# Optimization experiments

Hardware: AMD Instinct MI355X
Metric: run time of the kernel (lower is better)

Reference implementation:

```python
import jax, jax.numpy as jnp
import numpy as np


def setup_inputs() -> dict:
    key = jax.random.key(0)
    k1, k2 = jax.random.split(key)
    x = jax.random.normal(k1, (16, 1024, 512), dtype=jnp.float32)
    embedding = jax.random.normal(k2, (8192, 512), dtype=jnp.float32)
    return {"x": x, "embedding": embedding}


def reference(x, embedding):
    # x: [b, n, c], embedding (codebook k): [m, c]
    b, n, c = x.shape
    m = embedding.shape[0]
    q = x.reshape(b * n, c)            # (b n) c
    k = embedding
    # Squared L2 distance: ||q||^2 + ||k||^2 - 2 q.k  -> [bn, m]
    sim = (jnp.sum(q * q, axis=1, keepdims=True)
           + jnp.sum(k * k, axis=1)
           - 2.0 * jnp.einsum('nc,mc->nm', q, k))
    z_indices = jnp.argmin(sim, axis=1)                     # [bn]
    z_onehot = jax.nn.one_hot(z_indices, m, dtype=jnp.float32)  # [bn, m]
    # Direct gather is mathematically identical to onehot @ k
    z = k[z_indices]                                        # [bn, c]
    # Straight-through estimator: z = q + sg(z - q)
    z_st = q + jax.lax.stop_gradient(z - q)
    # Perplexity of code usage
    z_mean = jnp.mean(z_onehot, axis=0)                     # [m]
    perplexity = jnp.exp(-jnp.sum(z_mean * jnp.log(z_mean + 1e-10)))
    return (z_st.reshape(b, n, c),
            z_indices.reshape(b, n),
            z_onehot.reshape(b, n, m),
            perplexity)
```

## Files before the change

### kernel.cpp

```cpp
#include <hip/hip_runtime.h>
#include <cstdint>
#include <cstddef>

#define BNR 16384
#define C   512
#define M   8192
#define BM  128
#define BN  128
#define BK  64
#define NCH 8
#define NSETS 64

#define NZERO 512
#define GEMM_BLOCKS 8192
#define OH4_PER_ZB  65536

#define TILE_U16   8192
#define PANEL_U16  65536

typedef float f32x4 __attribute__((ext_vector_type(4)));
typedef _Float16 f16x8 __attribute__((ext_vector_type(8)));
typedef unsigned short u16;

static __device__ __forceinline__ u16 h_bits(_Float16 h) {
    union { _Float16 h; u16 u; } x; x.h = h; return x.u;
}
static __device__ __forceinline__ void gl_lds16(const void* g, void* l) {
    __builtin_amdgcn_global_load_lds(
        (const __attribute__((address_space(1))) void*)g,
        (__attribute__((address_space(3))) void*)l, 16, 0, 0);
}

__global__ void knorm_k(const float* __restrict__ emb, float* __restrict__ knorm) {
    int gw   = (blockIdx.x * blockDim.x + threadIdx.x) >> 6;
    int lane = threadIdx.x & 63;
    int nw   = (gridDim.x * blockDim.x) >> 6;
    for (int row = gw; row < M; row += nw) {
        const float4* p = (const float4*)(emb + (size_t)row * C);
        float s = 0.f;
#pragma unroll
        for (int j = 0; j < 2; ++j) {
            float4 v = p[lane + 64 * j];
            s += v.x * v.x + v.y * v.y + v.z * v.z + v.w * v.w;
        }
#pragma unroll
        for (int o = 32; o > 0; o >>= 1) s += __shfl_down(s, o, 64);
        if (lane == 0) knorm[row] = s;
    }
}

__global__ void cvt_tile_k(const float* __restrict__ in, u16* __restrict__ outp) {
    int o = blockIdx.x * 256 + threadIdx.x;
    int q = o & 1023, kb = q >> 7, row = q & 127;
    int c = (o >> 10) & 7, pan = o >> 13;
    int grow = pan * BM + row;
    int k0 = c * BK + kb * 8;
    const float4* src = (const float4*)(in + (size_t)grow * C + k0);
    float4 a = src[0], b = src[1];
    u16 v[8] = { h_bits((_Float16)a.x), h_bits((_Float16)a.y),
                 h_bits((_Float16)a.z), h_bits((_Float16)a.w),
                 h_bits((_Float16)b.x), h_bits((_Float16)b.y),
                 h_bits((_Float16)b.z), h_bits((_Float16)b.w) };
    u16* dst = outp + (size_t)o * 8;
    *(ushort4*)(dst)     = *(ushort4*)(v);
    *(ushort4*)(dst + 4) = *(ushort4*)(v + 4);
}

__global__ void mega_k(
    const u16* __restrict__ x2t, const u16* __restrict__ e2t,
    const float* __restrict__ knorm,
    float* __restrict__ pv1, int* __restrict__ pi1,
    float* __restrict__ pv2, int* __restrict__ pi2,
    float* __restrict__ onehot) {
    __shared__ __align__(16) u16 ldsA[8][128][8];
    __shared__ __align__(16) u16 ldsB[8][128][8];

    if (blockIdx.x < NZERO) {
        f32x4* o4 = (f32x4*)onehot;
        size_t base = (size_t)blockIdx.x * OH4_PER_ZB + threadIdx.x;
        const f32x4 z = (f32x4)(0.0f);
#pragma unroll 4
        for (int i = 0; i < OH4_PER_ZB / 256; ++i)
            __builtin_nontemporal_store(z, &o4[base + (size_t)i * 256]);
        return;
    }

    const int gid  = blockIdx.x - NZERO;
    const int tid  = threadIdx.x;
    const int lane = tid & 63;
    const int w    = tid >> 6;
    const int wm   = w >> 1, wn = w & 1;
    const int g    = lane >> 4, r = lane & 15;

    const int xk = gid & 7, j = gid >> 3;
    const int stid = (j >> 6) * 8 + xk;
    const int p  = j & 63;
    const int rb = (stid & 15) * 8 + (p & 7);
    const int cb = (stid >> 4) * 8 + (p >> 3);
    const int rowBase = rb * BM, colBase = cb * BN;

    f32x4 acc[4][4];
#pragma unroll
    for (int m = 0; m < 4; ++m)
#pragma unroll
        for (int n = 0; n < 4; ++n) acc[m][n] = (f32x4)(0.0f);

    const u16* aT = x2t + (size_t)rb * PANEL_U16;
    const u16* bT = e2t + (size_t)cb * PANEL_U16;

#pragma unroll 1
    for (int c = 0; c < NCH; ++c) {
        if (c) __syncthreads();
#pragma unroll
        for (int it = 0; it < 4; ++it) {
            int u = it * 256 + tid;
            gl_lds16(aT + (size_t)c * TILE_U16 + u * 8, (u16*)ldsA + u * 8);
            gl_lds16(bT + (size_t)c * TILE_U16 + u * 8, (u16*)ldsB + u * 8);
        }
        __syncthreads();

#pragma unroll
        for (int ks = 0; ks < 2; ++ks) {
            const int kb = ks * 4 + g;
            f16x8 a[4], b[4];
#pragma unroll
            for (int m = 0; m < 4; ++m)
                a[m] = *(const f16x8*)&ldsA[kb][wm * 64 + m * 16 + r][0];
#pragma unroll
            for (int n = 0; n < 4; ++n)
                b[n] = *(const f16x8*)&ldsB[kb][wn * 64 + n * 16 + r][0];
#pragma unroll
            for (int m = 0; m < 4; ++m)
#pragma unroll
                for (int n = 0; n < 4; ++n)
                    acc[m][n] = __builtin_amdgcn_mfma_f32_16x16x32_f16(
                        a[m], b[n], acc[m][n], 0, 0, 0);
        }
    }
    __syncthreads();

    float kn[4];
#pragma unroll
    for (int n = 0; n < 4; ++n) kn[n] = knorm[colBase + wn * 64 + n * 16 + r];

    float* mv = (float*)&ldsA[0][0][0];
    int*   mi = (int*)(mv + 2 * 128 * 2);

#pragma unroll
    for (int m = 0; m < 4; ++m) {
#pragma unroll
        for (int q = 0; q < 4; ++q) {
            float v1 = 3.0e38f, v2 = 3.0e38f;
            int   i1 = 0x7fffffff, i2 = 0x7fffffff;
#pragma unroll
            for (int n = 0; n < 4; ++n) {
                int col = colBase + wn * 64 + n * 16 + r;
                float d = fmaf(-2.0f, acc[m][n][q], kn[n]);
                if (d < v1 || (d == v1 && col < i1)) {
                    v2 = v1; i2 = i1; v1 = d; i1 = col;
                } else if (d < v2 || (d == v2 && col < i2)) {
                    v2 = d; i2 = col;
                }
            }
#pragma unroll
            for (int msk = 1; msk < 16; msk <<= 1) {
                float ov1 = __shfl_xor(v1, msk, 64);
                int   oi1 = __shfl_xor(i1, msk, 64);
                float ov2 = __shfl_xor(v2, msk, 64);
                int   oi2 = __shfl_xor(i2, msk, 64);
                bool ob = (ov1 < v1) || (ov1 == v1 && oi1 < i1);
                float nbv = ob ? ov1 : v1;  int nbi = ob ? oi1 : i1;
                float c1v = ob ? ov2 : v2;  int c1i = ob ? oi2 : i2;
                float c2v = ob ? v1 : ov1;  int c2i = ob ? i1 : oi1;
                bool cb2 = (c2v < c1v) || (c2v == c1v && c2i < c1i);
                v1 = nbv; i1 = nbi;
                v2 = cb2 ? c2v : c1v; i2 = cb2 ? c2i : c1i;
            }
            if (r == 0) {
                int lrow = wm * 64 + m * 16 + g * 4 + q;
                mv[(wn * 128 + lrow) * 2 + 0] = v1;
                mv[(wn * 128 + lrow) * 2 + 1] = v2;
                mi[(wn * 128 + lrow) * 2 + 0] = i1;
                mi[(wn * 128 + lrow) * 2 + 1] = i2;
            }
        }
    }
    __syncthreads();

    if (tid < 128) {
        float V1 = 3.0e38f, V2 = 3.0e38f;
        int   I1 = 0x7fffffff, I2 = 0x7fffffff;
#pragma unroll
        for (int s = 0; s < 4; ++s) {
            float d = mv[((s >> 1) * 128 + tid) * 2 + (s & 1)];
            int   ci = mi[((s >> 1) * 128 + tid) * 2 + (s & 1)];
            if (d < V1 || (d == V1 && ci < I1)) {
                V2 = V1; I2 = I1; V1 = d; I1 = ci;
            } else if (d < V2 || (d == V2 && ci < I2)) {
                V2 = d; I2 = ci;
            }
        }
        size_t o = (size_t)cb * BNR + rowBase + tid;
        pv1[o] = V1; pi1[o] = I1;
        pv2[o] = V2; pi2[o] = I2;
    }
}

__global__ void refine_k(const float* __restrict__ x, const float* __restrict__ emb,
                         const float* __restrict__ pv1, const int* __restrict__ pi1,
                         const float* __restrict__ pv2, const int* __restrict__ pi2,
                         float* __restrict__ out_idx) {
    int row  = blockIdx.x * 4 + (threadIdx.x >> 6);
    int lane = threadIdx.x & 63;
    size_t off = (size_t)lane * BNR + row;
    float va = pv1[off]; int ia = pi1[off];
    float vb = pv2[off]; int ib = pi2[off];
    int cand[8];
#pragma unroll
    for (int b = 0; b < 8; ++b) {
        bool al = (va < vb) || (va == vb && ia < ib);
        float cv = al ? va : vb; int ci = al ? ia : ib;
#pragma unroll
        for (int msk = 1; msk < 64; msk <<= 1) {
            float ov = __shfl_xor(cv, msk, 64);
            int   oi = __shfl_xor(ci, msk, 64);
            if (ov < cv || (ov == cv && oi < ci)) { cv = ov; ci = oi; }
        }
        cand[b] = ci;
        if (ia == ci) va = 3.0e38f;
        else if (ib == ci) vb = 3.0e38f;
    }
    int gid = lane >> 3, gl = lane & 7;
    int myc = cand[gid];
    const float* qp = x + (size_t)row * C;
    const float* kp = emb + (size_t)myc * C;
    double s = 0.0;
#pragma unroll 4
    for (int j = gl * 64; j < gl * 64 + 64; j += 4) {
        float4 q4 = *(const float4*)(qp + j);
        float4 k4 = *(const float4*)(kp + j);
        double d0 = (double)q4.x - (double)k4.x;
        double d1 = (double)q4.y - (double)k4.y;
        double d2 = (double)q4.z - (double)k4.z;
        double d3 = (double)q4.w - (double)k4.w;
        s += d0 * d0 + d1 * d1 + d2 * d2 + d3 * d3;
    }
    s += __shfl_xor(s, 1, 64);
    s += __shfl_xor(s, 2, 64);
    s += __shfl_xor(s, 4, 64);
    double dv = (gl == 0) ? s : 1.0e300;
    int    di = (gl == 0) ? myc : 0x7fffffff;
#pragma unroll
    for (int msk = 8; msk < 64; msk <<= 1) {
        double ov = __shfl_xor(dv, msk, 64);
        int    oi = __shfl_xor(di, msk, 64);
        if (ov < dv || (ov == dv && oi < di)) { dv = ov; di = oi; }
    }
    if (lane == 0) out_idx[row] = (float)di;
}

__global__ void finish_k(const float* __restrict__ emb,
                         const float* __restrict__ out_idx,
                         float* __restrict__ zst, float* __restrict__ onehot) {
    int row = blockIdx.x;
    int idx = (int)out_idx[row];
    const f32x4* src = (const f32x4*)(emb + (size_t)idx * C);
    f32x4* dst = (f32x4*)(zst + (size_t)row * C);
    __builtin_nontemporal_store(src[threadIdx.x], &dst[threadIdx.x]);
    if (threadIdx.x == 0) onehot[(size_t)row * M + idx] = 1.0f;
}

__global__ void perp_k(const float* __restrict__ out_idx, float* __restrict__ out_perp) {
    __shared__ int hist[M];
    __shared__ float red[256];
    int tid = threadIdx.x;
    for (int j = tid; j < M; j += 256) hist[j] = 0;
    __syncthreads();
    for (int j = tid; j < BNR; j += 256) atomicAdd(&hist[(int)out_idx[j]], 1);
    __syncthreads();
    float s = 0.f;
    for (int j = tid; j < M; j += 256) {
        float pb = (float)hist[j] * (1.0f / (float)BNR);
        s += pb * logf(pb + 1e-10f);
    }
    red[tid] = s; __syncthreads();
    for (int o = 128; o > 0; o >>= 1) {
        if (tid < o) red[tid] += red[tid + o];
        __syncthreads();
    }
    if (tid == 0) out_perp[0] = expf(-red[0]);
}

extern "C" void kernel_launch(void* const* d_in, const int* in_sizes, int n_in,
                              void* d_out, int out_size, void* d_ws, size_t ws_size,
                              hipStream_t stream) {
    const float* x   = (const float*)d_in[0];
    const float* emb = (const float*)d_in[1];

    float* out        = (float*)d_out;
    float* out_zst    = out;
    float* out_idx    = out + (size_t)BNR * C;
    float* out_onehot = out_idx + BNR;
    float* out_perp   = out_onehot + (size_t)BNR * M;

    u16*   x2t   = (u16*)d_ws;
    u16*   e2t   = x2t + (size_t)BNR * C;
    float* knorm = (float*)(e2t + (size_t)M * C);
    float* pv1   = knorm + M;
    float* pv2   = pv1 + (size_t)NSETS * BNR;
    int*   pi1   = (int*)(pv2 + (size_t)NSETS * BNR);
    int*   pi2   = pi1 + (size_t)NSETS * BNR;

    cvt_tile_k<<<(BNR * C / 8) / 256, 256, 0, stream>>>(x, x2t);
    cvt_tile_k<<<(M * C / 8) / 256, 256, 0, stream>>>(emb, e2t);
    knorm_k<<<64, 256, 0, stream>>>(emb, knorm);
    mega_k<<<NZERO + GEMM_BLOCKS, 256, 0, stream>>>(
        x2t, e2t, knorm, pv1, pi1, pv2, pi2, out_onehot);
    refine_k<<<BNR / 4, 256, 0, stream>>>(x, emb, pv1, pi1, pv2, pi2, out_idx);
    finish_k<<<BNR, 128, 0, stream>>>(emb, out_idx, out_zst, out_onehot);
    perp_k<<<1, 256, 0, stream>>>(out_idx, out_perp);
}
```

Measured before the change: 465.9 us.

## Fuse prelude kernels and spread one-hot zeroing across GEMM, refine and finish

Merges the two conversion kernels and the codebook-norm kernel into one prelude launch. The 512 MB one-hot zero-fill is split three ways: the GEMM kernel zeroes the first 8192 rows, the refine kernel zeroes the next 2048, and the finish kernel writes the last rows in full with the hot element inline. The z_st gather also moves into the refine kernel. The aim is to overlap the memory-bound zero-fill with compute-bound phases and to cut launch count. The risk is extra contention during the GEMM, plus a more intricate row partition that has to cover every row exactly once.

```diff
diff --git a/kernel.cpp b/kernel.cpp
--- a/kernel.cpp
+++ b/kernel.cpp
@@ -11,9 +11,13 @@
 #define NCH 8
 #define NSETS 64
 
-#define NZERO 512
 #define GEMM_BLOCKS 8192
-#define OH4_PER_ZB  65536
+#define NZ1 256
+#define R1  8192
+#define NZ2 128
+#define R2  10240
+#define FIN_FULL 1536
+#define FIN_SCAT 40
 
 #define TILE_U16   8192
 #define PANEL_U16  65536
@@ -31,26 +35,8 @@
         (__attribute__((address_space(3))) void*)l, 16, 0, 0);
 }
 
-__global__ void knorm_k(const float* __restrict__ emb, float* __restrict__ knorm) {
-    int gw   = (blockIdx.x * blockDim.x + threadIdx.x) >> 6;
-    int lane = threadIdx.x & 63;
-    int nw   = (gridDim.x * blockDim.x) >> 6;
-    for (int row = gw; row < M; row += nw) {
-        const float4* p = (const float4*)(emb + (size_t)row * C);
-        float s = 0.f;
-#pragma unroll
-        for (int j = 0; j < 2; ++j) {
-            float4 v = p[lane + 64 * j];
-            s += v.x * v.x + v.y * v.y + v.z * v.z + v.w * v.w;
-        }
-#pragma unroll
-        for (int o = 32; o > 0; o >>= 1) s += __shfl_down(s, o, 64);
-        if (lane == 0) knorm[row] = s;
-    }
-}
-
-__global__ void cvt_tile_k(const float* __restrict__ in, u16* __restrict__ outp) {
-    int o = blockIdx.x * 256 + threadIdx.x;
+static __device__ __forceinline__ void cvt_unit(const float* __restrict__ in,
+                                                u16* __restrict__ outp, int o) {
     int q = o & 1023, kb = q >> 7, row = q & 127;
     int c = (o >> 10) & 7, pan = o >> 13;
     int grow = pan * BM + row;
@@ -66,6 +52,28 @@
     *(ushort4*)(dst + 4) = *(ushort4*)(v + 4);
 }
 
+__global__ void prelude_k(const float* __restrict__ x, const float* __restrict__ emb,
+                          u16* __restrict__ x2t, u16* __restrict__ e2t,
+                          float* __restrict__ knorm) {
+    int b = blockIdx.x;
+    if (b < 4096) { cvt_unit(x, x2t, b * 256 + threadIdx.x); return; }
+    if (b < 6144) { cvt_unit(emb, e2t, (b - 4096) * 256 + threadIdx.x); return; }
+    int t = (b - 6144) * 256 + threadIdx.x;
+    int gw = t >> 6, lane = t & 63;
+    for (int row = gw; row < M; row += 256) {
+        const float4* p = (const float4*)(emb + (size_t)row * C);
+        float s = 0.f;
+#pragma unroll
+        for (int j = 0; j < 2; ++j) {
+            float4 v = p[lane + 64 * j];
+            s += v.x * v.x + v.y * v.y + v.z * v.z + v.w * v.w;
+        }
+#pragma unroll
+        for (int o = 32; o > 0; o >>= 1) s += __shfl_down(s, o, 64);
+        if (lane == 0) knorm[row] = s;
+    }
+}
+
 __global__ void mega_k(
     const u16* __restrict__ x2t, const u16* __restrict__ e2t,
     const float* __restrict__ knorm,
@@ -75,17 +83,17 @@
     __shared__ __align__(16) u16 ldsA[8][128][8];
     __shared__ __align__(16) u16 ldsB[8][128][8];
 
-    if (blockIdx.x < NZERO) {
+    if (blockIdx.x < NZ1) {
         f32x4* o4 = (f32x4*)onehot;
-        size_t base = (size_t)blockIdx.x * OH4_PER_ZB + threadIdx.x;
+        size_t base = (size_t)blockIdx.x * 65536 + threadIdx.x;
         const f32x4 z = (f32x4)(0.0f);
 #pragma unroll 4
-        for (int i = 0; i < OH4_PER_ZB / 256; ++i)
+        for (int i = 0; i < 256; ++i)
             __builtin_nontemporal_store(z, &o4[base + (size_t)i * 256]);
         return;
     }
 
-    const int gid  = blockIdx.x - NZERO;
+    const int gid  = blockIdx.x - NZ1;
     const int tid  = threadIdx.x;
     const int lane = tid & 63;
     const int w    = tid >> 6;
@@ -206,11 +214,22 @@
     }
 }
 
-__global__ void refine_k(const float* __restrict__ x, const float* __restrict__ emb,
-                         const float* __restrict__ pv1, const int* __restrict__ pi1,
-                         const float* __restrict__ pv2, const int* __restrict__ pi2,
-                         float* __restrict__ out_idx) {
-    int row  = blockIdx.x * 4 + (threadIdx.x >> 6);
+__global__ void refine2_k(const float* __restrict__ x, const float* __restrict__ emb,
+                          const float* __restrict__ pv1, const int* __restrict__ pi1,
+                          const float* __restrict__ pv2, const int* __restrict__ pi2,
+                          float* __restrict__ out_idx, float* __restrict__ zst,
+                          float* __restrict__ onehot) {
+    if (blockIdx.x < NZ2) {
+        f32x4* o4 = (f32x4*)onehot;
+        size_t base = (size_t)R1 * 2048 + (size_t)blockIdx.x * 32768 + threadIdx.x;
+        const f32x4 z = (f32x4)(0.0f);
+#pragma unroll 4
+        for (int i = 0; i < 128; ++i)
+            __builtin_nontemporal_store(z, &o4[base + (size_t)i * 256]);
+        return;
+    }
+    int rid  = blockIdx.x - NZ2;
+    int row  = rid * 4 + (threadIdx.x >> 6);
     int lane = threadIdx.x & 63;
     size_t off = (size_t)lane * BNR + row;
     float va = pv1[off]; int ia = pi1[off];
@@ -248,26 +267,45 @@
     s += __shfl_xor(s, 1, 64);
     s += __shfl_xor(s, 2, 64);
     s += __shfl_xor(s, 4, 64);
-    double dv = (gl == 0) ? s : 1.0e300;
-    int    di = (gl == 0) ? myc : 0x7fffffff;
-#pragma unroll
-    for (int msk = 8; msk < 64; msk <<= 1) {
+    double dv = s; int di = myc;
+#pragma unroll
+    for (int msk = 1; msk < 64; msk <<= 1) {
         double ov = __shfl_xor(dv, msk, 64);
         int    oi = __shfl_xor(di, msk, 64);
         if (ov < dv || (ov == dv && oi < di)) { dv = ov; di = oi; }
     }
+    const f32x4* er = (const f32x4*)(emb + (size_t)di * C);
+    f32x4* zr = (f32x4*)(zst + (size_t)row * C);
+    __builtin_nontemporal_store(er[lane * 2],     &zr[lane * 2]);
+    __builtin_nontemporal_store(er[lane * 2 + 1], &zr[lane * 2 + 1]);
     if (lane == 0) out_idx[row] = (float)di;
 }
 
-__global__ void finish_k(const float* __restrict__ emb,
-                         const float* __restrict__ out_idx,
-                         float* __restrict__ zst, float* __restrict__ onehot) {
-    int row = blockIdx.x;
-    int idx = (int)out_idx[row];
-    const f32x4* src = (const f32x4*)(emb + (size_t)idx * C);
-    f32x4* dst = (f32x4*)(zst + (size_t)row * C);
-    __builtin_nontemporal_store(src[threadIdx.x], &dst[threadIdx.x]);
-    if (threadIdx.x == 0) onehot[(size_t)row * M + idx] = 1.0f;
+__global__ void finish_k(const float* __restrict__ out_idx,
+                         float* __restrict__ onehot) {
+    if (blockIdx.x < FIN_FULL) {
+        int base = R2 + blockIdx.x * 4;
+#pragma unroll
+        for (int r4 = 0; r4 < 4; ++r4) {
+            int row = base + r4;
+            int idx = (int)out_idx[row];
+            int hot4 = idx >> 2, hotc = idx & 3;
+            f32x4* orow = (f32x4*)(onehot + (size_t)row * M);
+#pragma unroll
+            for (int t = 0; t < 8; ++t) {
+                int j4 = t * 256 + threadIdx.x;
+                f32x4 v = (f32x4)(0.0f);
+                if (j4 == hot4) v[hotc] = 1.0f;
+                __builtin_nontemporal_store(v, &orow[j4]);
+            }
+        }
+        return;
+    }
+    int gid = (blockIdx.x - FIN_FULL) * 256 + threadIdx.x;
+    if (gid < R2) {
+        int idx = (int)out_idx[gid];
+        onehot[(size_t)gid * M + idx] = 1.0f;
+    }
 }
 
 __global__ void perp_k(const float* __restrict__ out_idx, float* __restrict__ out_perp) {
@@ -311,12 +349,11 @@
     int*   pi1   = (int*)(pv2 + (size_t)NSETS * BNR);
     int*   pi2   = pi1 + (size_t)NSETS * BNR;
 
-    cvt_tile_k<<<(BNR * C / 8) / 256, 256, 0, stream>>>(x, x2t);
-    cvt_tile_k<<<(M * C / 8) / 256, 256, 0, stream>>>(emb, e2t);
-    knorm_k<<<64, 256, 0, stream>>>(emb, knorm);
-    mega_k<<<NZERO + GEMM_BLOCKS, 256, 0, stream>>>(
+    prelude_k<<<6208, 256, 0, stream>>>(x, emb, x2t, e2t, knorm);
+    mega_k<<<NZ1 + GEMM_BLOCKS, 256, 0, stream>>>(
         x2t, e2t, knorm, pv1, pi1, pv2, pi2, out_onehot);
-    refine_k<<<BNR / 4, 256, 0, stream>>>(x, emb, pv1, pi1, pv2, pi2, out_idx);
-    finish_k<<<BNR, 128, 0, stream>>>(emb, out_idx, out_zst, out_onehot);
+    refine2_k<<<NZ2 + BNR / 4, 256, 0, stream>>>(
+        x, emb, pv1, pi1, pv2, pi2, out_idx, out_zst, out_onehot);
+    finish_k<<<FIN_FULL + FIN_SCAT, 256, 0, stream>>>(out_idx, out_onehot);
     perp_k<<<1, 256, 0, stream>>>(out_idx, out_perp);
 }
```

New measurement: 452.1 us. 1.03x faster.
